# Performance work log

Measured on AMD Instinct MI355X. Metric: run time of the kernel, lower is better.

## Reference

```python
import jax, jax.numpy as jnp
import numpy as np

D_PARAM = 20   # module's d
S1 = 1         # module's s1
D_WIN = D_PARAM + S1   # 21: sliding-window size -> 441 displacement channels
PAD = D_PARAM // 2     # 10


def setup_inputs() -> dict:
    key = jax.random.key(0)
    k1, k2 = jax.random.split(key)
    B, C, W, H = 4, 128, 128, 128
    x1 = jax.random.normal(k1, (B, C, W, H), dtype=jnp.float32)
    x2 = jax.random.normal(k2, (B, C, W, H), dtype=jnp.float32)
    return {"x1": x1, "x2": x2}


def _correlation(x1, x2):
    # out[b, di*D+dj, i, j] = sum_c x1_padded[b, c, i+di, j+dj] * x2[b, c, i, j]
    # This reproduces: pad x1 by PAD, unfold 21x21 windows stride 1, and for each
    # pixel take the dot product over channels with x2[b,:,i,j] (the 1x1 conv2d
    # in the original triple loop). Flatten order of torch is (di, dj) row-major.
    b, c, w, h = x1.shape
    x1p = jnp.pad(x1, ((0, 0), (0, 0), (PAD, PAD), (PAD, PAD)))  # [b,c,w+20,h+20]
    rows_out = []
    for di in range(D_WIN):  # small fixed displacement loop (21 iters)
        rows = jax.lax.slice_in_dim(x1p, di, di + w, axis=2)  # [b,c,w,h+20]
        # stack 21 horizontal shifts -> [b,c,w,h,D_WIN]
        win = jnp.stack(
            [jax.lax.slice_in_dim(rows, dj, dj + h, axis=3) for dj in range(D_WIN)],
            axis=-1,
        )
        # contract over channels: [b, D_WIN(dj), w, h]
        rows_out.append(jnp.einsum('bcwhd,bcwh->bdwh', win, x2))
    out = jnp.stack(rows_out, axis=1)  # [b, D_WIN(di), D_WIN(dj), w, h]
    return out.reshape(b, D_WIN * D_WIN, w, h)


def reference(x1, x2):
    return _correlation(x1, x2)
```

## Files before the change

### kernel.cpp

```cpp
#include <hip/hip_runtime.h>


#define NB 4
#define NC 128
#define NW 128
#define NH 128
#define DW 21
#define PAD 10
#define NROW_T 148
#define NCOL_T 160
#define NCH 441
#define PS 37
#define SLICE_COLS 96
#define ROW_US (NCOL_T * NC)

typedef __attribute__((ext_vector_type(8))) short short8;
typedef __attribute__((ext_vector_type(4))) float float4v;

__device__ inline ushort f2bf(float f) {
    union { float f; uint u; } v; v.f = f;
    const uint u = v.u;
    return (ushort)((u + 0x7fffu + ((u >> 16) & 1u)) >> 16);
}

__device__ inline void async_copy16(const void* g, void* l) {
    __builtin_amdgcn_global_load_lds(
        (const __attribute__((address_space(1))) void*)g,
        (__attribute__((address_space(3))) void*)l, 16, 0, 0);
}

__global__ __launch_bounds__(256) void transpose_x1(const float* __restrict__ x1,
                                                    ushort* __restrict__ x1T) {
    __shared__ uint tile[128][65];
    const int t = threadIdx.x;
    const int b = blockIdx.x / NROW_T;
    const int r = blockIdx.x % NROW_T;
    const int w = r - PAD;
    const bool inr = (w >= 0 && w < NW);
    if (inr) {
        #pragma unroll
        for (int it = 0; it < 8; ++it) {
            const int u = it * 256 + t;
            const int g4 = u & 31;
            const int cp = u >> 5;
            const float4 va = *(const float4*)&x1[(((size_t)b * NC + 2 * cp    ) * NW + w) * NH + g4 * 4];
            const float4 vb = *(const float4*)&x1[(((size_t)b * NC + 2 * cp + 1) * NW + w) * NH + g4 * 4];
            tile[g4 * 4 + 0][cp] = (uint)f2bf(va.x) | ((uint)f2bf(vb.x) << 16);
            tile[g4 * 4 + 1][cp] = (uint)f2bf(va.y) | ((uint)f2bf(vb.y) << 16);
            tile[g4 * 4 + 2][cp] = (uint)f2bf(va.z) | ((uint)f2bf(vb.z) << 16);
            tile[g4 * 4 + 3][cp] = (uint)f2bf(va.w) | ((uint)f2bf(vb.w) << 16);
        }
    }
    __syncthreads();
    #pragma unroll
    for (int it = 0; it < 10; ++it) {
        const int u = it * 256 + t;
        const int cg = u & 15;
        const int col = u >> 4;
        uint4 v = make_uint4(0, 0, 0, 0);
        const int h = col - PAD;
        if (inr && h >= 0 && h < NH) {
            v.x = tile[h][cg * 4 + 0];
            v.y = tile[h][cg * 4 + 1];
            v.z = tile[h][cg * 4 + 2];
            v.w = tile[h][cg * 4 + 3];
        }
        const int chunk = cg ^ (col & 15);
        *(uint4*)&x1T[(((size_t)b * NROW_T + r) * NCOL_T + col) * NC + chunk * 8] = v;
    }
}

__global__ __launch_bounds__(256) void corr_mfma(const ushort* __restrict__ x1T,
                                                 const float* __restrict__ x2,
                                                 float* __restrict__ out) {
    __shared__ ushort win[2][SLICE_COLS * NC];
    __shared__ float patch[4][16 * PS];

    const int t = threadIdx.x;
    const int wave = t >> 6;
    const int lane = t & 63;
    const int n16 = lane & 15;
    const int q = lane >> 4;

    const int b = blockIdx.x >> 7;
    const int rem = blockIdx.x & 127;
    const int jhalf = rem & 1;
    const int i0 = (rem >> 1) * 2;

    const int ptile = wave >> 1;
    const int rowsel = wave & 1;
    const int i = i0 + rowsel;
    const int col0 = jhalf * 64;
    const int jbase = col0 + ptile * 32;

    short8 Bf[2][4];
    #pragma unroll
    for (int nt = 0; nt < 2; ++nt) {
        const int jc = jbase + nt * 16 + n16;
        #pragma unroll
        for (int k4 = 0; k4 < 4; ++k4) {
            short8 s;
            #pragma unroll
            for (int e = 0; e < 8; ++e) {
                const int c = k4 * 32 + q * 8 + e;
                s[e] = (short)f2bf(x2[(((size_t)b * NC + c) * NW + i) * NH + jc]);
            }
            Bf[nt][k4] = s;
        }
    }

    const ushort* x1Ts = x1T + (size_t)b * NROW_T * ROW_US + (size_t)col0 * NC;

    #pragma unroll
    for (int it = 0; it < 6; ++it) {
        const int off = it * 4096 + t * 16;
        async_copy16((const char*)(x1Ts + (size_t)(i0 + 0) * ROW_US) + off, (char*)win[0] + off);
        async_copy16((const char*)(x1Ts + (size_t)(i0 + 1) * ROW_US) + off, (char*)win[1] + off);
    }
    __syncthreads();

    float* P = &patch[wave][0];
    const int lcol = ptile * 32 + n16;

    for (int di = 0; di < DW; ++di) {
        const ushort* A = win[(di + rowsel) & 1];

        float4v a00 = {0.f,0.f,0.f,0.f}, a10 = {0.f,0.f,0.f,0.f}, a20 = {0.f,0.f,0.f,0.f};
        float4v a11 = {0.f,0.f,0.f,0.f}, a21 = {0.f,0.f,0.f,0.f}, a31 = {0.f,0.f,0.f,0.f};
        #pragma unroll
        for (int k4 = 0; k4 < 4; ++k4) {
            const int ch = (((q + 4 * k4) ^ n16) & 15) * 8;
            const short8 A0 = *(const short8*)&A[(lcol     ) * NC + ch];
            const short8 A1 = *(const short8*)&A[(lcol + 16) * NC + ch];
            const short8 A2 = *(const short8*)&A[(lcol + 32) * NC + ch];
            const short8 A3 = *(const short8*)&A[(lcol + 48) * NC + ch];
            a00 = __builtin_amdgcn_mfma_f32_16x16x32_bf16(A0, Bf[0][k4], a00, 0, 0, 0);
            a10 = __builtin_amdgcn_mfma_f32_16x16x32_bf16(A1, Bf[0][k4], a10, 0, 0, 0);
            a20 = __builtin_amdgcn_mfma_f32_16x16x32_bf16(A2, Bf[0][k4], a20, 0, 0, 0);
            a11 = __builtin_amdgcn_mfma_f32_16x16x32_bf16(A1, Bf[1][k4], a11, 0, 0, 0);
            a21 = __builtin_amdgcn_mfma_f32_16x16x32_bf16(A2, Bf[1][k4], a21, 0, 0, 0);
            a31 = __builtin_amdgcn_mfma_f32_16x16x32_bf16(A3, Bf[1][k4], a31, 0, 0, 0);
        }

        #pragma unroll
        for (int nt = 0; nt < 2; ++nt) {
            const float4v va = nt ? a11 : a00;
            const float4v vb = nt ? a21 : a10;
            const float4v vc = nt ? a31 : a20;
            #pragma unroll
            for (int reg = 0; reg < 4; ++reg) {
                P[n16 * PS + q * 4 + reg]      = va[reg];
                P[n16 * PS + 16 + q * 4 + reg] = vb[reg];
            }
            if (q == 0) {
                #pragma unroll
                for (int reg = 0; reg < 4; ++reg)
                    P[n16 * PS + 32 + reg] = vc[reg];
            }
            #pragma unroll
            for (int it2 = 0; it2 < 2; ++it2) {
                const int u = it2 * 64 + lane;
                if (u < 84) {
                    const int dj = u >> 2;
                    const int jj = (u & 3) * 4;
                    float4v v;
                    #pragma unroll
                    for (int p = 0; p < 4; ++p)
                        v[p] = P[(jj + p) * (PS + 1) + dj];
                    *(float4v*)&out[(((size_t)(b * NCH + di * DW + dj)) * NW + i) * NH
                                    + jbase + nt * 16 + jj] = v;
                }
            }
        }

        __syncthreads();
        if (di <= 19) {
            const char* src = (const char*)(x1Ts + (size_t)(i0 + di + 2) * ROW_US);
            char* dst = (char*)win[di & 1];
            #pragma unroll
            for (int it = 0; it < 6; ++it) {
                const int off = it * 4096 + t * 16;
                async_copy16(src + off, dst + off);
            }
        }
        __syncthreads();
    }
}

extern "C" void kernel_launch(void* const* d_in, const int* in_sizes, int n_in,
                              void* d_out, int out_size, void* d_ws, size_t ws_size,
                              hipStream_t stream) {
    const float* x1 = (const float*)d_in[0];
    const float* x2 = (const float*)d_in[1];
    float* out = (float*)d_out;
    ushort* x1T = (ushort*)d_ws;
    transpose_x1<<<dim3(NB * NROW_T), dim3(256), 0, stream>>>(x1, x1T);
    corr_mfma<<<dim3(NB * 128), dim3(256), 0, stream>>>(x1T, x2, out);
}
```

Before: 206.7 us.

## Retile correlation blocks to 4 rows x 32 cols with 4-deep row ring buffer

Each block now covers four output rows and a 32-column strip instead of two rows and 64 columns, and each wave owns one output row. The staged x1T window shrinks to 52 columns per row, kept in a four-slot LDS ring. The next row's async load is issued right after the MFMAs, so it overlaps the output transpose and stores. This cuts the redundant halo columns staged per block and moves the prefetch earlier. In exchange, more padded rows are reloaded across vertical neighbours, and the third-tile output selection changes to the q==3 lanes for the second column tile.

```diff
diff --git a/kernel.cpp b/kernel.cpp
--- a/kernel.cpp
+++ b/kernel.cpp
@@ -11,7 +11,8 @@
 #define NCOL_T 160
 #define NCH 441
 #define PS 37
-#define SLICE_COLS 96
+#define SCOLS 52
+#define SUS (SCOLS * NC)
 #define ROW_US (NCOL_T * NC)
 
 typedef __attribute__((ext_vector_type(8))) short short8;
@@ -27,6 +28,20 @@
     __builtin_amdgcn_global_load_lds(
         (const __attribute__((address_space(1))) void*)g,
         (__attribute__((address_space(3))) void*)l, 16, 0, 0);
+}
+
+__device__ inline void stage_row(const ushort* src, ushort* dst, int t) {
+    const char* s = (const char*)src;
+    char* d = (char*)dst;
+    #pragma unroll
+    for (int it = 0; it < 3; ++it) {
+        const int off = it * 4096 + t * 16;
+        async_copy16(s + off, d + off);
+    }
+    if (t < 64) {
+        const int off = 12288 + t * 16;
+        async_copy16(s + off, d + off);
+    }
 }
 
 __global__ __launch_bounds__(256) void transpose_x1(const float* __restrict__ x1,
@@ -73,7 +88,7 @@
 __global__ __launch_bounds__(256) void corr_mfma(const ushort* __restrict__ x1T,
                                                  const float* __restrict__ x2,
                                                  float* __restrict__ out) {
-    __shared__ ushort win[2][SLICE_COLS * NC];
+    __shared__ ushort win[4][SUS];
     __shared__ float patch[4][16 * PS];
 
     const int t = threadIdx.x;
@@ -84,19 +99,22 @@
 
     const int b = blockIdx.x >> 7;
     const int rem = blockIdx.x & 127;
-    const int jhalf = rem & 1;
-    const int i0 = (rem >> 1) * 2;
-
-    const int ptile = wave >> 1;
-    const int rowsel = wave & 1;
-    const int i = i0 + rowsel;
-    const int col0 = jhalf * 64;
-    const int jbase = col0 + ptile * 32;
+    const int jq = rem & 3;
+    const int iq = rem >> 2;
+    const int i0 = iq * 4;
+    const int col0 = jq * 32;
+    const int i = i0 + wave;
+
+    const ushort* xbase = x1T + (size_t)(b * NROW_T) * ROW_US + (size_t)col0 * NC;
+
+    #pragma unroll
+    for (int r = 0; r < 4; ++r)
+        stage_row(xbase + (size_t)(i0 + r) * ROW_US, win[r], t);
 
     short8 Bf[2][4];
     #pragma unroll
     for (int nt = 0; nt < 2; ++nt) {
-        const int jc = jbase + nt * 16 + n16;
+        const int jc = col0 + nt * 16 + n16;
         #pragma unroll
         for (int k4 = 0; k4 < 4; ++k4) {
             short8 s;
@@ -109,50 +127,49 @@
         }
     }
 
-    const ushort* x1Ts = x1T + (size_t)b * NROW_T * ROW_US + (size_t)col0 * NC;
-
-    #pragma unroll
-    for (int it = 0; it < 6; ++it) {
-        const int off = it * 4096 + t * 16;
-        async_copy16((const char*)(x1Ts + (size_t)(i0 + 0) * ROW_US) + off, (char*)win[0] + off);
-        async_copy16((const char*)(x1Ts + (size_t)(i0 + 1) * ROW_US) + off, (char*)win[1] + off);
-    }
     __syncthreads();
 
     float* P = &patch[wave][0];
-    const int lcol = ptile * 32 + n16;
 
     for (int di = 0; di < DW; ++di) {
-        const ushort* A = win[(di + rowsel) & 1];
-
-        float4v a00 = {0.f,0.f,0.f,0.f}, a10 = {0.f,0.f,0.f,0.f}, a20 = {0.f,0.f,0.f,0.f};
-        float4v a11 = {0.f,0.f,0.f,0.f}, a21 = {0.f,0.f,0.f,0.f}, a31 = {0.f,0.f,0.f,0.f};
+        const ushort* A = win[(di + wave) & 3];
+
+        float4v a00 = {0.f,0.f,0.f,0.f}, a01 = {0.f,0.f,0.f,0.f}, a02 = {0.f,0.f,0.f,0.f};
+        float4v a10 = {0.f,0.f,0.f,0.f}, a11 = {0.f,0.f,0.f,0.f}, a12 = {0.f,0.f,0.f,0.f};
         #pragma unroll
         for (int k4 = 0; k4 < 4; ++k4) {
-            const int ch = (((q + 4 * k4) ^ n16) & 15) * 8;
-            const short8 A0 = *(const short8*)&A[(lcol     ) * NC + ch];
-            const short8 A1 = *(const short8*)&A[(lcol + 16) * NC + ch];
-            const short8 A2 = *(const short8*)&A[(lcol + 32) * NC + ch];
-            const short8 A3 = *(const short8*)&A[(lcol + 48) * NC + ch];
+            const int kc = q + 4 * k4;
+            const int c0 = (0  + n16);
+            const int c1 = (16 + n16);
+            const int c2 = (32 + n16);
+            const int c3 = (36 + n16);
+            const short8 A0 = *(const short8*)&A[c0 * NC + ((kc ^ (c0 & 15)) & 15) * 8];
+            const short8 A1 = *(const short8*)&A[c1 * NC + ((kc ^ (c1 & 15)) & 15) * 8];
+            const short8 A2 = *(const short8*)&A[c2 * NC + ((kc ^ (c2 & 15)) & 15) * 8];
+            const short8 A3 = *(const short8*)&A[c3 * NC + ((kc ^ (c3 & 15)) & 15) * 8];
             a00 = __builtin_amdgcn_mfma_f32_16x16x32_bf16(A0, Bf[0][k4], a00, 0, 0, 0);
-            a10 = __builtin_amdgcn_mfma_f32_16x16x32_bf16(A1, Bf[0][k4], a10, 0, 0, 0);
-            a20 = __builtin_amdgcn_mfma_f32_16x16x32_bf16(A2, Bf[0][k4], a20, 0, 0, 0);
-            a11 = __builtin_amdgcn_mfma_f32_16x16x32_bf16(A1, Bf[1][k4], a11, 0, 0, 0);
-            a21 = __builtin_amdgcn_mfma_f32_16x16x32_bf16(A2, Bf[1][k4], a21, 0, 0, 0);
-            a31 = __builtin_amdgcn_mfma_f32_16x16x32_bf16(A3, Bf[1][k4], a31, 0, 0, 0);
-        }
+            a01 = __builtin_amdgcn_mfma_f32_16x16x32_bf16(A1, Bf[0][k4], a01, 0, 0, 0);
+            a02 = __builtin_amdgcn_mfma_f32_16x16x32_bf16(A2, Bf[0][k4], a02, 0, 0, 0);
+            a10 = __builtin_amdgcn_mfma_f32_16x16x32_bf16(A1, Bf[1][k4], a10, 0, 0, 0);
+            a11 = __builtin_amdgcn_mfma_f32_16x16x32_bf16(A2, Bf[1][k4], a11, 0, 0, 0);
+            a12 = __builtin_amdgcn_mfma_f32_16x16x32_bf16(A3, Bf[1][k4], a12, 0, 0, 0);
+        }
+
+        __syncthreads();
+        if (di < DW - 1)
+            stage_row(xbase + (size_t)(i0 + di + 4) * ROW_US, win[di & 3], t);
 
         #pragma unroll
         for (int nt = 0; nt < 2; ++nt) {
-            const float4v va = nt ? a11 : a00;
-            const float4v vb = nt ? a21 : a10;
-            const float4v vc = nt ? a31 : a20;
+            const float4v va = nt ? a10 : a00;
+            const float4v vb = nt ? a11 : a01;
+            const float4v vc = nt ? a12 : a02;
             #pragma unroll
             for (int reg = 0; reg < 4; ++reg) {
                 P[n16 * PS + q * 4 + reg]      = va[reg];
                 P[n16 * PS + 16 + q * 4 + reg] = vb[reg];
             }
-            if (q == 0) {
+            if (q == (nt ? 3 : 0)) {
                 #pragma unroll
                 for (int reg = 0; reg < 4; ++reg)
                     P[n16 * PS + 32 + reg] = vc[reg];
@@ -168,21 +185,11 @@
                     for (int p = 0; p < 4; ++p)
                         v[p] = P[(jj + p) * (PS + 1) + dj];
                     *(float4v*)&out[(((size_t)(b * NCH + di * DW + dj)) * NW + i) * NH
-                                    + jbase + nt * 16 + jj] = v;
+                                    + col0 + nt * 16 + jj] = v;
                 }
             }
         }
 
-        __syncthreads();
-        if (di <= 19) {
-            const char* src = (const char*)(x1Ts + (size_t)(i0 + di + 2) * ROW_US);
-            char* dst = (char*)win[di & 1];
-            #pragma unroll
-            for (int it = 0; it < 6; ++it) {
-                const int off = it * 4096 + t * 16;
-                async_copy16(src + off, dst + off);
-            }
-        }
         __syncthreads();
     }
 }
@@ -195,5 +202,5 @@
     float* out = (float*)d_out;
     ushort* x1T = (ushort*)d_ws;
     transpose_x1<<<dim3(NB * NROW_T), dim3(256), 0, stream>>>(x1, x1T);
-    corr_mfma<<<dim3(NB * 128), dim3(256), 0, stream>>>(x1T, x2, out);
-}
+    corr_mfma<<<dim3(NB * 32 * 4), dim3(256), 0, stream>>>(x1T, x2, out);
+}
```

Result: faster. 194.4 us (-5.9%).
